# Performance work log

Measured on AMD Instinct MI355X. Metric: run time of the kernel, lower is better.

Reference implementation:

```python
import jax, jax.numpy as jnp
import numpy as np


def setup_inputs() -> dict:
    key = jax.random.key(0)
    k1, k2, k3, k4, k5 = jax.random.split(key, 5)
    N, L, V = 8, 2048, 512
    E = 2 * V
    tokens = jax.random.randint(k1, (N, L, E), 0, 2, dtype=jnp.int64)
    s = 1.0 / np.sqrt(E)
    Wa_w = jax.random.uniform(k2, (E, E), jnp.float32, -s, s)
    Wa_b = jax.random.uniform(k3, (E,), jnp.float32, -s, s)
    Wb_w = jax.random.uniform(k4, (V, E), jnp.float32, -s, s)
    Wb_b = jax.random.uniform(k5, (V,), jnp.float32, -s, s)
    return {"tokens": tokens, "Wa_w": Wa_w, "Wa_b": Wa_b, "Wb_w": Wb_w, "Wb_b": Wb_b}


def reference(tokens, Wa_w, Wa_b, Wb_w, Wb_b):
    # x: [N, L, E] float embedding of binary tokens
    x = tokens.astype(jnp.float32)
    # q = Wa(x): [N, L, E] (torch Linear: x @ W^T + b)
    q = jnp.einsum("nle,fe->nlf", x, Wa_w) + Wa_b
    # scores: [N, L, L]; softmax over last dim
    scores = jnp.einsum("nlf,nmf->nlm", q, x)
    wts = jax.nn.softmax(scores, axis=-1)
    # a = wts @ x: [N, L, E]
    a = jnp.einsum("nlm,nme->nle", wts, x)
    # y = Wb(a): [N, L, V]; logits from last position
    y = jnp.einsum("nle,ve->nlv", a, Wb_w) + Wb_b
    logits = y[:, -1]  # [N, V]
    return logits
```

## Files before the change

### kernel.cpp

```cpp
#include <hip/hip_runtime.h>

#define NB 8
#define LS 2048
#define ED 1024
#define VD 512
#define CH 32
#define CM 64

__device__ inline float wave_reduce_sum(float v) {
    #pragma unroll
    for (int off = 32; off > 0; off >>= 1)
        v += __shfl_down(v, off, 64);
    return v;
}

__global__ void k_qrow(const int* __restrict__ tokens, const float* __restrict__ Wa_w,
                       const float* __restrict__ Wa_b, float* __restrict__ q_row) {
    int wid  = blockIdx.x * (blockDim.x >> 6) + (threadIdx.x >> 6);
    int lane = threadIdx.x & 63;
    int n = wid >> 10;
    int f = wid & (ED - 1);
    const int*   xrow = tokens + ((size_t)n * LS + (LS - 1)) * ED;
    const float* wrow = Wa_w + (size_t)f * ED;
    float acc = 0.f;
    #pragma unroll
    for (int k = 0; k < ED; k += 256) {
        int idx = k + lane * 4;
        int4   t = *reinterpret_cast<const int4*>(xrow + idx);
        float4 w = *reinterpret_cast<const float4*>(wrow + idx);
        acc += (float)t.x * w.x + (float)t.y * w.y + (float)t.z * w.z + (float)t.w * w.w;
    }
    acc = wave_reduce_sum(acc);
    if (lane == 0) q_row[wid] = acc + Wa_b[f];
}

__global__ __launch_bounds__(1024) void k_flash(const int* __restrict__ tokens,
                                                const float* __restrict__ q_row,
                                                float* __restrict__ pa,
                                                float* __restrict__ mu_g,
                                                float* __restrict__ z_g) {
    int n = blockIdx.x >> 5;
    int c = blockIdx.x & (CH - 1);
    int t = threadIdx.x;
    int wave = t >> 6, lane = t & 63;

    __shared__ unsigned long long pk[CM][16];
    __shared__ float s_lds[CM];
    __shared__ float p_lds[CM];
    __shared__ float red[4][ED];

    const float* q = q_row + n * ED;

    #pragma unroll
    for (int i = 0; i < 4; ++i) {
        int m = wave + 16 * i;
        const int* row = tokens + ((size_t)(n * LS + c * CM + m)) * ED;
        float acc = 0.f;
        #pragma unroll
        for (int k = 0; k < ED; k += 256) {
            int idx = k + lane * 4;
            int4   tv = *reinterpret_cast<const int4*>(row + idx);
            float4 qv = *reinterpret_cast<const float4*>(q + idx);
            unsigned long long b0 = __ballot(tv.x != 0);
            unsigned long long b1 = __ballot(tv.y != 0);
            unsigned long long b2 = __ballot(tv.z != 0);
            unsigned long long b3 = __ballot(tv.w != 0);
            if (lane == 0) {
                int wb = (k >> 8) * 4;
                pk[m][wb + 0] = b0; pk[m][wb + 1] = b1;
                pk[m][wb + 2] = b2; pk[m][wb + 3] = b3;
            }
            acc += (float)tv.x * qv.x + (float)tv.y * qv.y
                 + (float)tv.z * qv.z + (float)tv.w * qv.w;
        }
        acc = wave_reduce_sum(acc);
        if (lane == 0) s_lds[m] = acc;
    }
    __syncthreads();

    if (wave == 0) {
        float s = s_lds[lane];
        float mx = s;
        #pragma unroll
        for (int off = 32; off > 0; off >>= 1) mx = fmaxf(mx, __shfl_xor(mx, off, 64));
        float p = expf(s - mx);
        float zz = p;
        #pragma unroll
        for (int off = 32; off > 0; off >>= 1) zz += __shfl_xor(zz, off, 64);
        p_lds[lane] = p;
        if (lane == 0) { mu_g[n * CH + c] = mx; z_g[n * CH + c] = zz; }
    }
    __syncthreads();

    int mg  = t >> 8;
    int e4  = t & 255;
    int wb  = (e4 >> 6) * 4;
    int bit = e4 & 63;
    float a0 = 0.f, a1 = 0.f, a2 = 0.f, a3 = 0.f;
    #pragma unroll
    for (int j = 0; j < 16; ++j) {
        int m = mg + 4 * j;
        float p = p_lds[m];
        unsigned long long w0 = pk[m][wb + 0];
        unsigned long long w1 = pk[m][wb + 1];
        unsigned long long w2 = pk[m][wb + 2];
        unsigned long long w3 = pk[m][wb + 3];
        a0 += ((w0 >> bit) & 1ull) ? p : 0.f;
        a1 += ((w1 >> bit) & 1ull) ? p : 0.f;
        a2 += ((w2 >> bit) & 1ull) ? p : 0.f;
        a3 += ((w3 >> bit) & 1ull) ? p : 0.f;
    }
    *reinterpret_cast<float4*>(&red[mg][e4 * 4]) = make_float4(a0, a1, a2, a3);
    __syncthreads();

    float s4 = red[0][t] + red[1][t] + red[2][t] + red[3][t];
    pa[((size_t)(n * CH + c)) * ED + t] = s4;
}

__global__ __launch_bounds__(1024) void k_combine(const float* __restrict__ pa,
                                                  const float* __restrict__ mu_g,
                                                  const float* __restrict__ z_g,
                                                  float* __restrict__ a_row) {
    int n = blockIdx.x;
    int t = threadIdx.x;
    __shared__ float coef[CH];
    __shared__ float invZ_s;
    if (t < 64) {
        float m_c = (t < CH) ? mu_g[n * CH + t] : -3.0e38f;
        float mx = m_c;
        #pragma unroll
        for (int off = 32; off > 0; off >>= 1) mx = fmaxf(mx, __shfl_xor(mx, off, 64));
        float cf = (t < CH) ? expf(m_c - mx) : 0.f;
        float zc = (t < CH) ? z_g[n * CH + t] * cf : 0.f;
        float Z = zc;
        #pragma unroll
        for (int off = 32; off > 0; off >>= 1) Z += __shfl_xor(Z, off, 64);
        if (t < CH) coef[t] = cf;
        if (t == 0) invZ_s = 1.f / Z;
    }
    __syncthreads();
    float inv = invZ_s;
    float acc = 0.f;
    #pragma unroll
    for (int ci = 0; ci < CH; ++ci)
        acc += coef[ci] * pa[((size_t)(n * CH + ci)) * ED + t];
    a_row[n * ED + t] = acc * inv;
}

__global__ void k_out(const float* __restrict__ a_row, const float* __restrict__ Wb_w,
                      const float* __restrict__ Wb_b, float* __restrict__ out) {
    int wid  = blockIdx.x * (blockDim.x >> 6) + (threadIdx.x >> 6);
    int lane = threadIdx.x & 63;
    int n = wid >> 9;
    int v = wid & (VD - 1);
    const float* a  = a_row + n * ED;
    const float* wr = Wb_w + (size_t)v * ED;
    float acc = 0.f;
    #pragma unroll
    for (int k = 0; k < ED; k += 256) {
        int idx = k + lane * 4;
        float4 av = *reinterpret_cast<const float4*>(a + idx);
        float4 wv = *reinterpret_cast<const float4*>(wr + idx);
        acc += av.x * wv.x + av.y * wv.y + av.z * wv.z + av.w * wv.w;
    }
    acc = wave_reduce_sum(acc);
    if (lane == 0) out[wid] = acc + Wb_b[v];
}

extern "C" void kernel_launch(void* const* d_in, const int* in_sizes, int n_in,
                              void* d_out, int out_size, void* d_ws, size_t ws_size,
                              hipStream_t stream) {
    const int*   tokens = (const int*)  d_in[0];
    const float* Wa_w   = (const float*)d_in[1];
    const float* Wa_b   = (const float*)d_in[2];
    const float* Wb_w   = (const float*)d_in[3];
    const float* Wb_b   = (const float*)d_in[4];
    float* out = (float*)d_out;

    float* ws    = (float*)d_ws;
    float* q_row = ws;
    float* pa    = q_row + NB * ED;
    float* mu_g  = pa + (size_t)NB * CH * ED;
    float* z_g   = mu_g + NB * CH;
    float* a_row = z_g + NB * CH;

    k_qrow<<<dim3((NB * ED) / 4), dim3(256), 0, stream>>>(tokens, Wa_w, Wa_b, q_row);
    k_flash<<<dim3(NB * CH), dim3(1024), 0, stream>>>(tokens, q_row, pa, mu_g, z_g);
    k_combine<<<dim3(NB), dim3(1024), 0, stream>>>(pa, mu_g, z_g, a_row);
    k_out<<<dim3((NB * VD) / 4), dim3(256), 0, stream>>>(a_row, Wb_w, Wb_b, out);
}
```

Baseline: 30.83 us.

## Split flash pass into score/pack and weighted-sum kernels, fuse combine into output

```diff
diff --git a/kernel.cpp b/kernel.cpp
--- a/kernel.cpp
+++ b/kernel.cpp
@@ -6,6 +6,7 @@
 #define VD 512
 #define CH 32
 #define CM 64
+typedef unsigned long long u64;
 
 __device__ inline float wave_reduce_sum(float v) {
     #pragma unroll
@@ -34,137 +35,105 @@
     if (lane == 0) q_row[wid] = acc + Wa_b[f];
 }
 
-__global__ __launch_bounds__(1024) void k_flash(const int* __restrict__ tokens,
-                                                const float* __restrict__ q_row,
-                                                float* __restrict__ pa,
-                                                float* __restrict__ mu_g,
-                                                float* __restrict__ z_g) {
-    int n = blockIdx.x >> 5;
-    int c = blockIdx.x & (CH - 1);
-    int t = threadIdx.x;
-    int wave = t >> 6, lane = t & 63;
-
-    __shared__ unsigned long long pk[CM][16];
-    __shared__ float s_lds[CM];
-    __shared__ float p_lds[CM];
-    __shared__ float red[4][ED];
-
-    const float* q = q_row + n * ED;
-
-    #pragma unroll
-    for (int i = 0; i < 4; ++i) {
-        int m = wave + 16 * i;
-        const int* row = tokens + ((size_t)(n * LS + c * CM + m)) * ED;
-        float acc = 0.f;
-        #pragma unroll
-        for (int k = 0; k < ED; k += 256) {
-            int idx = k + lane * 4;
-            int4   tv = *reinterpret_cast<const int4*>(row + idx);
-            float4 qv = *reinterpret_cast<const float4*>(q + idx);
-            unsigned long long b0 = __ballot(tv.x != 0);
-            unsigned long long b1 = __ballot(tv.y != 0);
-            unsigned long long b2 = __ballot(tv.z != 0);
-            unsigned long long b3 = __ballot(tv.w != 0);
-            if (lane == 0) {
-                int wb = (k >> 8) * 4;
-                pk[m][wb + 0] = b0; pk[m][wb + 1] = b1;
-                pk[m][wb + 2] = b2; pk[m][wb + 3] = b3;
-            }
-            acc += (float)tv.x * qv.x + (float)tv.y * qv.y
-                 + (float)tv.z * qv.z + (float)tv.w * qv.w;
-        }
-        acc = wave_reduce_sum(acc);
-        if (lane == 0) s_lds[m] = acc;
-    }
-    __syncthreads();
-
-    if (wave == 0) {
-        float s = s_lds[lane];
-        float mx = s;
-        #pragma unroll
-        for (int off = 32; off > 0; off >>= 1) mx = fmaxf(mx, __shfl_xor(mx, off, 64));
-        float p = expf(s - mx);
-        float zz = p;
-        #pragma unroll
-        for (int off = 32; off > 0; off >>= 1) zz += __shfl_xor(zz, off, 64);
-        p_lds[lane] = p;
-        if (lane == 0) { mu_g[n * CH + c] = mx; z_g[n * CH + c] = zz; }
-    }
-    __syncthreads();
-
-    int mg  = t >> 8;
-    int e4  = t & 255;
-    int wb  = (e4 >> 6) * 4;
-    int bit = e4 & 63;
-    float a0 = 0.f, a1 = 0.f, a2 = 0.f, a3 = 0.f;
-    #pragma unroll
-    for (int j = 0; j < 16; ++j) {
-        int m = mg + 4 * j;
-        float p = p_lds[m];
-        unsigned long long w0 = pk[m][wb + 0];
-        unsigned long long w1 = pk[m][wb + 1];
-        unsigned long long w2 = pk[m][wb + 2];
-        unsigned long long w3 = pk[m][wb + 3];
-        a0 += ((w0 >> bit) & 1ull) ? p : 0.f;
-        a1 += ((w1 >> bit) & 1ull) ? p : 0.f;
-        a2 += ((w2 >> bit) & 1ull) ? p : 0.f;
-        a3 += ((w3 >> bit) & 1ull) ? p : 0.f;
-    }
-    *reinterpret_cast<float4*>(&red[mg][e4 * 4]) = make_float4(a0, a1, a2, a3);
-    __syncthreads();
-
-    float s4 = red[0][t] + red[1][t] + red[2][t] + red[3][t];
-    pa[((size_t)(n * CH + c)) * ED + t] = s4;
-}
-
-__global__ __launch_bounds__(1024) void k_combine(const float* __restrict__ pa,
-                                                  const float* __restrict__ mu_g,
-                                                  const float* __restrict__ z_g,
-                                                  float* __restrict__ a_row) {
-    int n = blockIdx.x;
-    int t = threadIdx.x;
-    __shared__ float coef[CH];
-    __shared__ float invZ_s;
-    if (t < 64) {
-        float m_c = (t < CH) ? mu_g[n * CH + t] : -3.0e38f;
-        float mx = m_c;
-        #pragma unroll
-        for (int off = 32; off > 0; off >>= 1) mx = fmaxf(mx, __shfl_xor(mx, off, 64));
-        float cf = (t < CH) ? expf(m_c - mx) : 0.f;
-        float zc = (t < CH) ? z_g[n * CH + t] * cf : 0.f;
-        float Z = zc;
-        #pragma unroll
-        for (int off = 32; off > 0; off >>= 1) Z += __shfl_xor(Z, off, 64);
-        if (t < CH) coef[t] = cf;
-        if (t == 0) invZ_s = 1.f / Z;
-    }
-    __syncthreads();
-    float inv = invZ_s;
-    float acc = 0.f;
-    #pragma unroll
-    for (int ci = 0; ci < CH; ++ci)
-        acc += coef[ci] * pa[((size_t)(n * CH + ci)) * ED + t];
-    a_row[n * ED + t] = acc * inv;
-}
-
-__global__ void k_out(const float* __restrict__ a_row, const float* __restrict__ Wb_w,
-                      const float* __restrict__ Wb_b, float* __restrict__ out) {
+__global__ void k_scorepack(const int* __restrict__ tokens, const float* __restrict__ q_row,
+                            float* __restrict__ scores, u64* __restrict__ pk) {
     int wid  = blockIdx.x * (blockDim.x >> 6) + (threadIdx.x >> 6);
     int lane = threadIdx.x & 63;
-    int n = wid >> 9;
-    int v = wid & (VD - 1);
-    const float* a  = a_row + n * ED;
-    const float* wr = Wb_w + (size_t)v * ED;
+    int n = wid >> 11;
+    int m = wid & (LS - 1);
+    const int*   xrow = tokens + (size_t)wid * ED;
+    const float* q    = q_row + n * ED;
+    u64* pkrow = pk + (size_t)wid * 16;
     float acc = 0.f;
     #pragma unroll
     for (int k = 0; k < ED; k += 256) {
         int idx = k + lane * 4;
-        float4 av = *reinterpret_cast<const float4*>(a + idx);
-        float4 wv = *reinterpret_cast<const float4*>(wr + idx);
-        acc += av.x * wv.x + av.y * wv.y + av.z * wv.z + av.w * wv.w;
+        int4   tv = *reinterpret_cast<const int4*>(xrow + idx);
+        float4 qv = *reinterpret_cast<const float4*>(q + idx);
+        u64 b0 = __ballot(tv.x != 0);
+        u64 b1 = __ballot(tv.y != 0);
+        u64 b2 = __ballot(tv.z != 0);
+        u64 b3 = __ballot(tv.w != 0);
+        u64 bb = b0;
+        bb = (lane == 1) ? b1 : bb;
+        bb = (lane == 2) ? b2 : bb;
+        bb = (lane == 3) ? b3 : bb;
+        if (lane < 4) pkrow[(k >> 6) + lane] = bb;
+        acc += (float)tv.x * qv.x + (float)tv.y * qv.y
+             + (float)tv.z * qv.z + (float)tv.w * qv.w;
     }
     acc = wave_reduce_sum(acc);
-    if (lane == 0) out[wid] = acc + Wb_b[v];
+    if (lane == 0) scores[wid] = acc;
+}
+
+__global__ __launch_bounds__(1024) void k_wsum(const float* __restrict__ scores,
+                                               const u64* __restrict__ pk,
+                                               float* __restrict__ partial) {
+    int n = blockIdx.x >> 5;
+    int c = blockIdx.x & (CH - 1);
+    int t = threadIdx.x;
+    __shared__ float red[1024];
+    __shared__ float p_lds[CM];
+
+    float s0 = scores[n * LS + t];
+    float s1 = scores[n * LS + t + 1024];
+    red[t] = fmaxf(s0, s1); __syncthreads();
+    for (int off = 512; off > 0; off >>= 1) {
+        if (t < off) red[t] = fmaxf(red[t], red[t + off]);
+        __syncthreads();
+    }
+    float mu = red[0]; __syncthreads();
+    red[t] = expf(s0 - mu) + expf(s1 - mu); __syncthreads();
+    for (int off = 512; off > 0; off >>= 1) {
+        if (t < off) red[t] += red[t + off];
+        __syncthreads();
+    }
+    float invZ = 1.f / red[0];
+    if (t < CM) p_lds[t] = expf(scores[n * LS + c * CM + t] - mu) * invZ;
+    __syncthreads();
+
+    const u64* rows = pk + ((size_t)(n * LS + c * CM)) * 16;
+    int w   = ((t >> 8) << 2) | (t & 3);
+    int bit = (t >> 2) & 63;
+    float acc = 0.f;
+    #pragma unroll 8
+    for (int m = 0; m < CM; ++m) {
+        acc += ((rows[m * 16 + w] >> bit) & 1ull) ? p_lds[m] : 0.f;
+    }
+    partial[(size_t)blockIdx.x * ED + t] = acc;
+}
+
+__global__ __launch_bounds__(1024) void k_out(const float* __restrict__ partial,
+                                              const float* __restrict__ Wb_w,
+                                              const float* __restrict__ Wb_b,
+                                              float* __restrict__ out) {
+    int n  = blockIdx.x >> 4;
+    int vt = blockIdx.x & 15;
+    int t  = threadIdx.x;
+    int wave = t >> 6, lane = t & 63;
+    __shared__ float a_lds[ED];
+
+    float acc = 0.f;
+    #pragma unroll
+    for (int c = 0; c < CH; ++c)
+        acc += partial[((size_t)(n * CH + c)) * ED + t];
+    a_lds[t] = acc; __syncthreads();
+
+    #pragma unroll
+    for (int i = 0; i < 2; ++i) {
+        int v = vt * 32 + wave * 2 + i;
+        const float* wr = Wb_w + (size_t)v * ED;
+        float d = 0.f;
+        #pragma unroll
+        for (int k = 0; k < ED; k += 256) {
+            int idx = k + lane * 4;
+            float4 wv = *reinterpret_cast<const float4*>(wr + idx);
+            float4 av = *reinterpret_cast<const float4*>(&a_lds[idx]);
+            d += av.x * wv.x + av.y * wv.y + av.z * wv.z + av.w * wv.w;
+        }
+        d = wave_reduce_sum(d);
+        if (lane == 0) out[n * VD + v] = d + Wb_b[v];
+    }
 }
 
 extern "C" void kernel_launch(void* const* d_in, const int* in_sizes, int n_in,
@@ -177,15 +146,13 @@
     const float* Wb_b   = (const float*)d_in[4];
     float* out = (float*)d_out;
 
-    float* ws    = (float*)d_ws;
-    float* q_row = ws;
-    float* pa    = q_row + NB * ED;
-    float* mu_g  = pa + (size_t)NB * CH * ED;
-    float* z_g   = mu_g + NB * CH;
-    float* a_row = z_g + NB * CH;
+    u64*   pk      = (u64*)d_ws;
+    float* q_row   = (float*)(pk + (size_t)NB * LS * 16);
+    float* scores  = q_row + NB * ED;
+    float* partial = scores + NB * LS;
 
     k_qrow<<<dim3((NB * ED) / 4), dim3(256), 0, stream>>>(tokens, Wa_w, Wa_b, q_row);
-    k_flash<<<dim3(NB * CH), dim3(1024), 0, stream>>>(tokens, q_row, pa, mu_g, z_g);
-    k_combine<<<dim3(NB), dim3(1024), 0, stream>>>(pa, mu_g, z_g, a_row);
-    k_out<<<dim3((NB * VD) / 4), dim3(256), 0, stream>>>(a_row, Wb_w, Wb_b, out);
+    k_scorepack<<<dim3((NB * LS) / 4), dim3(256), 0, stream>>>(tokens, q_row, scores, pk);
+    k_wsum<<<dim3(NB * CH), dim3(1024), 0, stream>>>(scores, pk, partial);
+    k_out<<<dim3(NB * 16), dim3(1024), 0, stream>>>(partial, Wb_w, Wb_b, out);
 }
```

Result: slower. 51.23 us (+66.2%).
